# Kernel optimization log

Measured on AMD Instinct MI355X. Metric: run time of the kernel, lower is better.

The kernel has to match this reference:

```python
import jax, jax.numpy as jnp
import numpy as np

N = 50000
SELF_LOOP_W = 2.0  # GCNConv(improved=True)


def gcn_conv(x, edge_index, W, b):
    # x: [N, Fin], edge_index: [2, E] (row=source, col=target)
    h = x @ W  # [N, Fout]
    row, col = edge_index[0], edge_index[1]
    ones = jnp.ones(row.shape[0], dtype=h.dtype)
    deg = jax.ops.segment_sum(ones, col, num_segments=N) + SELF_LOOP_W
    dinv = jnp.where(deg > 0, jax.lax.rsqrt(deg), 0.0)
    norm = dinv[row] * dinv[col]  # [E]
    agg = jax.ops.segment_sum(norm[:, None] * h[row], col, num_segments=N)
    # self-loop contribution: weight 2.0, norm = dinv[i]^2
    agg = agg + (SELF_LOOP_W * dinv * dinv)[:, None] * h
    return agg + b


def setup_inputs() -> dict:
    key = jax.random.key(0)
    ks = jax.random.split(key, 12)
    F_in, H1, H2, H3 = 256, 256, 128, 64
    E, Ep, En = 800000, 200000, 200000
    def glorot(k, shape):
        lim = np.sqrt(6.0 / (shape[0] + shape[1]))
        return jax.random.uniform(k, shape, jnp.float32, -lim, lim)
    return {
        "x": jax.random.normal(ks[0], (N, F_in), jnp.float32),
        "train_edge_index": jax.random.randint(ks[1], (2, E), 0, N),
        "pos_edge_index": jax.random.randint(ks[2], (2, Ep), 0, N),
        "neg_edge_index": jax.random.randint(ks[3], (2, En), 0, N),
        "W1": glorot(ks[4], (F_in, H1)),
        "b1": jnp.zeros((H1,), jnp.float32),
        "W2": glorot(ks[5], (H1, H2)),
        "b2": jnp.zeros((H2,), jnp.float32),
        "Wl1": glorot(ks[6], (H2, H3)),
        "bl1": jnp.zeros((H3,), jnp.float32),
        "Wl2": glorot(ks[7], (H3, 1)),
        "bl2": jnp.zeros((1,), jnp.float32),
    }


def reference(x, train_edge_index, pos_edge_index, neg_edge_index,
              W1, b1, W2, b2, Wl1, bl1, Wl2, bl2):
    h = jax.nn.relu(gcn_conv(x, train_edge_index, W1, b1))
    h = gcn_conv(h, train_edge_index, W2, b2)  # [N, 128]
    tei = jnp.concatenate([pos_edge_index, neg_edge_index], axis=-1)  # [2, Ep+En]
    e = h[tei[1]] + h[tei[0]]  # x_i + x_j, [Etot, 128]
    e = jax.nn.relu(e @ Wl1 + bl1)
    e = jax.nn.sigmoid(e @ Wl2 + bl2)
    return e.reshape(-1)
```

## Files before the change

kernel.cpp:

```cpp
#include <hip/hip_runtime.h>
#include <math.h>

#define NV 50000
#define ETR 800000
#define EPOS 200000
#define ETEST 400000

typedef __attribute__((ext_vector_type(8))) short bf16x8;
typedef __attribute__((ext_vector_type(8))) unsigned short ushortx8;
typedef __attribute__((ext_vector_type(4))) float f32x4;

__device__ inline unsigned short f2b(float f) {
    union { float f; unsigned u; } v; v.f = f;
    unsigned r = v.u + 0x7fffu + ((v.u >> 16) & 1u);
    return (unsigned short)(r >> 16);
}
__device__ inline float blo(unsigned q) { union { unsigned u; float f; } v; v.u = q << 16; return v.f; }
__device__ inline float bhi(unsigned q) { union { unsigned u; float f; } v; v.u = q & 0xffff0000u; return v.f; }
__device__ inline float b2f(unsigned short s) { union { unsigned u; float f; } v; v.u = ((unsigned)s) << 16; return v.f; }

__device__ inline ushortx8 bf16add8(ushortx8 a, ushortx8 b) {
    ushortx8 r;
    #pragma unroll
    for (int i = 0; i < 8; ++i)
        r[i] = f2b(b2f(a[i]) + b2f(b[i]));
    return r;
}


__global__ void deg_kernel(const int* __restrict__ tei, int* __restrict__ deg) {
    int e = blockIdx.x * blockDim.x + threadIdx.x;
    if (e < ETR) atomicAdd(&deg[tei[ETR + e]], 1);
}

__global__ __launch_bounds__(1024) void partial_kernel(const int* __restrict__ deg,
                                                       int* __restrict__ partials) {
    int i = blockIdx.x * 1024 + threadIdx.x;
    int v = (i < NV) ? deg[i] : 0;
    #pragma unroll
    for (int off = 32; off > 0; off >>= 1) v += __shfl_xor(v, off);
    __shared__ int wsum[16];
    if ((threadIdx.x & 63) == 0) wsum[threadIdx.x >> 6] = v;
    __syncthreads();
    if (threadIdx.x == 0) {
        int s = 0;
        #pragma unroll
        for (int k = 0; k < 16; ++k) s += wsum[k];
        partials[blockIdx.x] = s;
    }
}

__global__ __launch_bounds__(1024) void ptr_kernel(
    const int* __restrict__ deg, const int* __restrict__ partials,
    int* __restrict__ ptr, int* __restrict__ cursor, float* __restrict__ dinv)
{
    int b = blockIdx.x, t = threadIdx.x;
    int i = b * 1024 + t;
    int d = (i < NV) ? deg[i] : 0;
    int lane = t & 63, w = t >> 6;
    int v = d;
    #pragma unroll
    for (int off = 1; off < 64; off <<= 1) {
        int u = __shfl_up(v, off);
        if (lane >= off) v += u;
    }
    __shared__ int wsum[16], woff[16];
    if (lane == 63) wsum[w] = v;
    __syncthreads();
    if (t == 0) {
        int s = 0;
        for (int k = 0; k < b; ++k) s += partials[k];
        for (int k = 0; k < 16; ++k) { woff[k] = s; s += wsum[k]; }
    }
    __syncthreads();
    int excl = woff[w] + v - d;
    if (i < NV) {
        ptr[i] = excl;
        cursor[i] = excl;
        dinv[i] = rsqrtf((float)d + 2.0f);
        if (i == NV - 1) ptr[NV] = excl + d;
    }
}

__global__ void fill_kernel(const int* __restrict__ tei, const float* __restrict__ dinv,
                            int* __restrict__ cursor, int2* __restrict__ edat) {
    int e = blockIdx.x * blockDim.x + threadIdx.x;
    if (e < ETR) {
        int row = tei[e];
        int col = tei[ETR + e];
        int p = atomicAdd(&cursor[col], 1);
        edat[p] = make_int2(row, __float_as_int(dinv[row] * dinv[col]));
    }
}


__global__ void cvt_wt_all_kernel(const float* __restrict__ W1, const float* __restrict__ W2,
                                  const float* __restrict__ Wl1,
                                  unsigned short* __restrict__ w1t, unsigned short* __restrict__ w2t,
                                  unsigned short* __restrict__ wl1t) {
    int idx = blockIdx.x * blockDim.x + threadIdx.x;
    if (idx < 65536) {
        int n = idx >> 8, k = idx & 255;
        w1t[idx] = f2b(W1[k * 256 + n]);
    } else if (idx < 98304) {
        int i = idx - 65536;
        int n = i >> 8, k = i & 255;
        w2t[i] = f2b(W2[k * 128 + n]);
    } else if (idx < 106496) {
        int i = idx - 98304;
        int n = i >> 7, k = i & 127;
        wl1t[i] = f2b(Wl1[k * 64 + n]);
    }
}


template<int N, int K, bool AF32>
__global__ __launch_bounds__(256) void mfma_gemm_kernel(
    const void* __restrict__ Av, const unsigned short* __restrict__ Bt,
    unsigned short* __restrict__ C, int M)
{
    constexpr int BK = 64;
    __shared__ unsigned short Asm[128][BK];
    __shared__ unsigned short Bsm[128][BK];
    int tid = threadIdx.x;
    int lane = tid & 63, wid = tid >> 6;
    int wr = wid >> 1, wc = wid & 1;
    int row0 = blockIdx.x * 128, col0 = blockIdx.y * 128;

    int sr = tid >> 3;
    int s8 = tid & 7;
    int sswz = s8 ^ (sr & 7);
    int fr = lane & 15;
    int g  = lane >> 4;

    f32x4 acc[4][4] = {};

    for (int k0 = 0; k0 < K; k0 += BK) {
        #pragma unroll
        for (int i = 0; i < 4; ++i) {
            int r = sr + i * 32;
            int gr = row0 + r;
            ushortx8 va = {0, 0, 0, 0, 0, 0, 0, 0};
            if constexpr (AF32) {
                const float* Af = (const float*)Av;
                if (gr < M) {
                    float4 f0 = *(const float4*)&Af[(size_t)gr * K + k0 + s8 * 8];
                    float4 f1 = *(const float4*)&Af[(size_t)gr * K + k0 + s8 * 8 + 4];
                    va[0] = f2b(f0.x); va[1] = f2b(f0.y); va[2] = f2b(f0.z); va[3] = f2b(f0.w);
                    va[4] = f2b(f1.x); va[5] = f2b(f1.y); va[6] = f2b(f1.z); va[7] = f2b(f1.w);
                }
            } else {
                const unsigned short* Ab = (const unsigned short*)Av;
                if (gr < M) va = *(const ushortx8*)&Ab[(size_t)gr * K + k0 + s8 * 8];
            }
            *(ushortx8*)&Asm[r][sswz * 8] = va;
            ushortx8 vb = *(const ushortx8*)&Bt[(size_t)(col0 + r) * K + k0 + s8 * 8];
            *(ushortx8*)&Bsm[r][sswz * 8] = vb;
        }
        __syncthreads();
        #pragma unroll
        for (int kf = 0; kf < BK; kf += 32) {
            int sbase = kf >> 3;
            bf16x8 af[4], bfr[4];
            #pragma unroll
            for (int m = 0; m < 4; ++m) {
                int rr = wr * 64 + m * 16 + fr;
                af[m] = *(const bf16x8*)&Asm[rr][((sbase + g) ^ (fr & 7)) * 8];
            }
            #pragma unroll
            for (int n = 0; n < 4; ++n) {
                int rr = wc * 64 + n * 16 + fr;
                bfr[n] = *(const bf16x8*)&Bsm[rr][((sbase + g) ^ (fr & 7)) * 8];
            }
            #pragma unroll
            for (int m = 0; m < 4; ++m)
                #pragma unroll
                for (int n = 0; n < 4; ++n)
                    acc[m][n] = __builtin_amdgcn_mfma_f32_16x16x32_bf16(af[m], bfr[n], acc[m][n], 0, 0, 0);
        }
        __syncthreads();
    }

    #pragma unroll
    for (int m = 0; m < 4; ++m) {
        int rbase = row0 + wr * 64 + m * 16 + g * 4;
        #pragma unroll
        for (int j = 0; j < 4; ++j) {
            int r = rbase + j;
            if (r < M) {
                #pragma unroll
                for (int n = 0; n < 4; ++n) {
                    int c = col0 + wc * 64 + n * 16 + fr;
                    C[(size_t)r * N + c] = f2b(acc[m][n][j]);
                }
            }
        }
    }
}


template<int F, bool RELU>
__global__ __launch_bounds__(256) void gather_kernel(
    const int* __restrict__ ptr, const int2* __restrict__ edat,
    const float* __restrict__ dinv, const unsigned short* __restrict__ hlin,
    const float* __restrict__ bias, unsigned short* __restrict__ hout)
{
    constexpr int V = F / 64;
    int gid = blockIdx.x * blockDim.x + threadIdx.x;
    int node = gid >> 6, lane = gid & 63;
    if (node >= NV) return;
    float dc = dinv[node];
    int j0 = ptr[node], j1 = ptr[node + 1];
    float acc[V] = {};
    const unsigned short* hb = hlin + lane * V;
    const long long* edl = (const long long*)edat;

    int j = j0;
    for (; j + 7 < j1; j += 8) {
        long long e[8];
        #pragma unroll
        for (int u = 0; u < 8; ++u) e[u] = __builtin_nontemporal_load(edl + j + u);
        if constexpr (V == 4) {
            uint2 q[8];
            #pragma unroll
            for (int u = 0; u < 8; ++u)
                q[u] = *(const uint2*)(hb + (size_t)(int)e[u] * F);
            #pragma unroll
            for (int u = 0; u < 8; ++u) {
                float n = __int_as_float((int)(e[u] >> 32));
                acc[0] += n * blo(q[u].x);
                acc[1] += n * bhi(q[u].x);
                acc[2] += n * blo(q[u].y);
                acc[3] += n * bhi(q[u].y);
            }
        } else {
            unsigned q[8];
            #pragma unroll
            for (int u = 0; u < 8; ++u)
                q[u] = *(const unsigned*)(hb + (size_t)(int)e[u] * F);
            #pragma unroll
            for (int u = 0; u < 8; ++u) {
                float n = __int_as_float((int)(e[u] >> 32));
                acc[0] += n * blo(q[u]);
                acc[1] += n * bhi(q[u]);
            }
        }
    }
    for (; j + 3 < j1; j += 4) {
        long long e[4];
        #pragma unroll
        for (int u = 0; u < 4; ++u) e[u] = __builtin_nontemporal_load(edl + j + u);
        if constexpr (V == 4) {
            uint2 q[4];
            #pragma unroll
            for (int u = 0; u < 4; ++u)
                q[u] = *(const uint2*)(hb + (size_t)(int)e[u] * F);
            #pragma unroll
            for (int u = 0; u < 4; ++u) {
                float n = __int_as_float((int)(e[u] >> 32));
                acc[0] += n * blo(q[u].x);
                acc[1] += n * bhi(q[u].x);
                acc[2] += n * blo(q[u].y);
                acc[3] += n * bhi(q[u].y);
            }
        } else {
            unsigned q[4];
            #pragma unroll
            for (int u = 0; u < 4; ++u)
                q[u] = *(const unsigned*)(hb + (size_t)(int)e[u] * F);
            #pragma unroll
            for (int u = 0; u < 4; ++u) {
                float n = __int_as_float((int)(e[u] >> 32));
                acc[0] += n * blo(q[u]);
                acc[1] += n * bhi(q[u]);
            }
        }
    }
    for (; j < j1; ++j) {
        long long e0 = __builtin_nontemporal_load(edl + j);
        float n0 = __int_as_float((int)(e0 >> 32));
        if constexpr (V == 4) {
            uint2 q0 = *(const uint2*)(hb + (size_t)(int)e0 * F);
            acc[0] += n0 * blo(q0.x);
            acc[1] += n0 * bhi(q0.x);
            acc[2] += n0 * blo(q0.y);
            acc[3] += n0 * bhi(q0.y);
        } else {
            unsigned q0 = *(const unsigned*)(hb + (size_t)(int)e0 * F);
            acc[0] += n0 * blo(q0);
            acc[1] += n0 * bhi(q0);
        }
    }

    const unsigned short* ps = hb + (size_t)node * F;
    float sw = 2.0f * dc * dc;
    if constexpr (V == 4) {
        uint2 qs = *(const uint2*)ps;
        float o0 = acc[0] + sw * blo(qs.x) + bias[lane * 4 + 0];
        float o1 = acc[1] + sw * bhi(qs.x) + bias[lane * 4 + 1];
        float o2 = acc[2] + sw * blo(qs.y) + bias[lane * 4 + 2];
        float o3 = acc[3] + sw * bhi(qs.y) + bias[lane * 4 + 3];
        if (RELU) {
            o0 = fmaxf(o0, 0.f); o1 = fmaxf(o1, 0.f);
            o2 = fmaxf(o2, 0.f); o3 = fmaxf(o3, 0.f);
        }
        union { unsigned short u[4]; unsigned long long ll; } pk;
        pk.u[0] = f2b(o0); pk.u[1] = f2b(o1); pk.u[2] = f2b(o2); pk.u[3] = f2b(o3);
        __builtin_nontemporal_store(pk.ll, (unsigned long long*)(hout + (size_t)node * F + lane * 4));
    } else {
        unsigned qs = *(const unsigned*)ps;
        float o0 = acc[0] + sw * blo(qs) + bias[lane * 2 + 0];
        float o1 = acc[1] + sw * bhi(qs) + bias[lane * 2 + 1];
        if (RELU) { o0 = fmaxf(o0, 0.f); o1 = fmaxf(o1, 0.f); }
        union { unsigned short u[2]; unsigned q; } pk;
        pk.u[0] = f2b(o0); pk.u[1] = f2b(o1);
        __builtin_nontemporal_store(pk.q, (unsigned*)(hout + (size_t)node * F + lane * 2));
    }
}


__global__ __launch_bounds__(256) void edge_mlp_mfma_kernel(
    const int* __restrict__ pos, const int* __restrict__ neg,
    const unsigned short* __restrict__ h2, const unsigned short* __restrict__ Wl1t,
    const float* __restrict__ bl1, const float* __restrict__ Wl2,
    const float* __restrict__ bl2, float* __restrict__ out)
{
    __shared__ unsigned short Es[128][128];
    __shared__ unsigned short Ws[64][128];
    int tid = threadIdx.x;
    int lane = tid & 63, w = tid >> 6;
    int fr = lane & 15, g = lane >> 4;
    int e0 = blockIdx.x * 128;

    #pragma unroll
    for (int k = 0; k < 4; ++k) {
        int chunk = tid + k * 256;
        int row = chunk >> 4, c = chunk & 15;
        *(ushortx8*)&Ws[row][(c ^ (row & 7)) * 8] = *(const ushortx8*)&Wl1t[chunk * 8];
    }

    int et = tid >> 1, hh = tid & 1;
    int eg = e0 + et;
    int a, b;
    if (eg < EPOS) { a = pos[eg]; b = pos[EPOS + eg]; }
    else { int i = eg - EPOS; a = neg[i]; b = neg[EPOS + i]; }
    const unsigned short* pa = h2 + (size_t)a * 128 + hh * 64;
    const unsigned short* pb = h2 + (size_t)b * 128 + hh * 64;
    #pragma unroll
    for (int c8 = 0; c8 < 8; ++c8) {
        ushortx8 va = *(const ushortx8*)&pa[c8 * 8];
        ushortx8 vb = *(const ushortx8*)&pb[c8 * 8];
        ushortx8 vs = bf16add8(va, vb);
        int c = hh * 8 + c8;
        *(ushortx8*)&Es[et][(c ^ (et & 7)) * 8] = vs;
    }
    __syncthreads();

    f32x4 acc[2][4] = {};
    #pragma unroll
    for (int ks = 0; ks < 4; ++ks) {
        int c = ks * 4 + g;
        bf16x8 af[2], bfr[4];
        #pragma unroll
        for (int m = 0; m < 2; ++m) {
            int r = w * 32 + m * 16 + fr;
            af[m] = *(const bf16x8*)&Es[r][(c ^ (r & 7)) * 8];
        }
        #pragma unroll
        for (int n = 0; n < 4; ++n) {
            int r = n * 16 + fr;
            bfr[n] = *(const bf16x8*)&Ws[r][(c ^ (r & 7)) * 8];
        }
        #pragma unroll
        for (int m = 0; m < 2; ++m)
            #pragma unroll
            for (int n = 0; n < 4; ++n)
                acc[m][n] = __builtin_amdgcn_mfma_f32_16x16x32_bf16(af[m], bfr[n], acc[m][n], 0, 0, 0);
    }

    float bl2v = bl2[0];
    float b1v[4], w2v[4];
    #pragma unroll
    for (int n = 0; n < 4; ++n) {
        b1v[n] = bl1[n * 16 + fr];
        w2v[n] = Wl2[n * 16 + fr];
    }
    #pragma unroll
    for (int m = 0; m < 2; ++m) {
        float p[4];
        #pragma unroll
        for (int j = 0; j < 4; ++j) {
            float s = 0.f;
            #pragma unroll
            for (int n = 0; n < 4; ++n)
                s += fmaxf(acc[m][n][j] + b1v[n], 0.0f) * w2v[n];
            p[j] = s;
        }
        #pragma unroll
        for (int off = 1; off < 16; off <<= 1) {
            #pragma unroll
            for (int j = 0; j < 4; ++j)
                p[j] += __shfl_xor(p[j], off);
        }
        int ebase = e0 + w * 32 + m * 16 + g * 4;
        #pragma unroll
        for (int j = 0; j < 4; ++j)
            if (fr == j)
                out[ebase + j] = 1.0f / (1.0f + expf(-(p[j] + bl2v)));
    }
}


extern "C" void kernel_launch(void* const* d_in, const int* in_sizes, int n_in,
                              void* d_out, int out_size, void* d_ws, size_t ws_size,
                              hipStream_t stream) {
    const float* x   = (const float*)d_in[0];
    const int*   tei = (const int*)d_in[1];
    const int*   pos = (const int*)d_in[2];
    const int*   neg = (const int*)d_in[3];
    const float* W1  = (const float*)d_in[4];
    const float* b1  = (const float*)d_in[5];
    const float* W2  = (const float*)d_in[6];
    const float* b2  = (const float*)d_in[7];
    const float* Wl1 = (const float*)d_in[8];
    const float* bl1 = (const float*)d_in[9];
    const float* Wl2 = (const float*)d_in[10];
    const float* bl2 = (const float*)d_in[11];
    float* out = (float*)d_out;

    float* fws = (float*)d_ws;
    int*   iws = (int*)d_ws;
    unsigned short* usws = (unsigned short*)d_ws;
    float* dinv     = fws;
    int*   deg      = iws + 50000;
    int*   ptr      = iws + 100000;
    int*   cursor   = iws + 150002;
    int2*  edat     = (int2*)(iws + 200064);
    int*   partials = iws + 1800064;
    unsigned short* w1t  = usws + 2ull * 1800192;
    unsigned short* w2t  = usws + 2ull * 1832960;
    unsigned short* wl1t = usws + 2ull * 1849344;
    unsigned short* bufX = usws + 2ull * 1853504;
    unsigned short* bufL16 = usws + 2ull * 8253504;
    unsigned short* bufH = usws + 2ull * 14653504;

    hipMemsetAsync(deg, 0, NV * sizeof(int), stream);

    deg_kernel<<<(ETR + 255) / 256, 256, 0, stream>>>(tei, deg);
    partial_kernel<<<49, 1024, 0, stream>>>(deg, partials);
    ptr_kernel<<<49, 1024, 0, stream>>>(deg, partials, ptr, cursor, dinv);
    fill_kernel<<<(ETR + 255) / 256, 256, 0, stream>>>(tei, dinv, cursor, edat);
    cvt_wt_all_kernel<<<416, 256, 0, stream>>>(W1, W2, Wl1, w1t, w2t, wl1t);

    mfma_gemm_kernel<256, 256, true><<<dim3(391, 2), 256, 0, stream>>>(x, w1t, bufL16, NV);
    gather_kernel<256, true><<<(NV * 64) / 256, 256, 0, stream>>>(ptr, edat, dinv, bufL16, b1, bufH);

    mfma_gemm_kernel<128, 256, false><<<dim3(391, 1), 256, 0, stream>>>(bufH, w2t, bufX, NV);
    gather_kernel<128, false><<<(NV * 64) / 256, 256, 0, stream>>>(ptr, edat, dinv, bufX, b2, bufL16);

    edge_mlp_mfma_kernel<<<ETEST / 128, 256, 0, stream>>>(pos, neg, bufL16, wl1t, bl1, Wl2, bl2, out);
}
```

Baseline: 298.1 us.

## Merge independent preprocessing kernels into combined block-partitioned launches

Folds the degree atomic count and the W1 transpose/convert into one launch, and folds the first GEMM, the degree partial sums and the W2/Wl1 conversions into a second launch, with blocks dispatched by block index. This cuts the kernel count from eleven to eight, removing launch gaps and letting the small independent tasks share the machine with the GEMM. Costs: the merged kernels carry the GEMM's shared memory and register footprint for every block, and partial sums now run alongside the GEMM rather than before it.

Result: faster. 291.7 us (-2.1%).

```diff
diff --git a/kernel.cpp b/kernel.cpp
--- a/kernel.cpp
+++ b/kernel.cpp
@@ -28,96 +28,10 @@
 }
 
 
-__global__ void deg_kernel(const int* __restrict__ tei, int* __restrict__ deg) {
-    int e = blockIdx.x * blockDim.x + threadIdx.x;
-    if (e < ETR) atomicAdd(&deg[tei[ETR + e]], 1);
-}
-
-__global__ __launch_bounds__(1024) void partial_kernel(const int* __restrict__ deg,
-                                                       int* __restrict__ partials) {
-    int i = blockIdx.x * 1024 + threadIdx.x;
-    int v = (i < NV) ? deg[i] : 0;
-    #pragma unroll
-    for (int off = 32; off > 0; off >>= 1) v += __shfl_xor(v, off);
-    __shared__ int wsum[16];
-    if ((threadIdx.x & 63) == 0) wsum[threadIdx.x >> 6] = v;
-    __syncthreads();
-    if (threadIdx.x == 0) {
-        int s = 0;
-        #pragma unroll
-        for (int k = 0; k < 16; ++k) s += wsum[k];
-        partials[blockIdx.x] = s;
-    }
-}
-
-__global__ __launch_bounds__(1024) void ptr_kernel(
-    const int* __restrict__ deg, const int* __restrict__ partials,
-    int* __restrict__ ptr, int* __restrict__ cursor, float* __restrict__ dinv)
-{
-    int b = blockIdx.x, t = threadIdx.x;
-    int i = b * 1024 + t;
-    int d = (i < NV) ? deg[i] : 0;
-    int lane = t & 63, w = t >> 6;
-    int v = d;
-    #pragma unroll
-    for (int off = 1; off < 64; off <<= 1) {
-        int u = __shfl_up(v, off);
-        if (lane >= off) v += u;
-    }
-    __shared__ int wsum[16], woff[16];
-    if (lane == 63) wsum[w] = v;
-    __syncthreads();
-    if (t == 0) {
-        int s = 0;
-        for (int k = 0; k < b; ++k) s += partials[k];
-        for (int k = 0; k < 16; ++k) { woff[k] = s; s += wsum[k]; }
-    }
-    __syncthreads();
-    int excl = woff[w] + v - d;
-    if (i < NV) {
-        ptr[i] = excl;
-        cursor[i] = excl;
-        dinv[i] = rsqrtf((float)d + 2.0f);
-        if (i == NV - 1) ptr[NV] = excl + d;
-    }
-}
-
-__global__ void fill_kernel(const int* __restrict__ tei, const float* __restrict__ dinv,
-                            int* __restrict__ cursor, int2* __restrict__ edat) {
-    int e = blockIdx.x * blockDim.x + threadIdx.x;
-    if (e < ETR) {
-        int row = tei[e];
-        int col = tei[ETR + e];
-        int p = atomicAdd(&cursor[col], 1);
-        edat[p] = make_int2(row, __float_as_int(dinv[row] * dinv[col]));
-    }
-}
-
-
-__global__ void cvt_wt_all_kernel(const float* __restrict__ W1, const float* __restrict__ W2,
-                                  const float* __restrict__ Wl1,
-                                  unsigned short* __restrict__ w1t, unsigned short* __restrict__ w2t,
-                                  unsigned short* __restrict__ wl1t) {
-    int idx = blockIdx.x * blockDim.x + threadIdx.x;
-    if (idx < 65536) {
-        int n = idx >> 8, k = idx & 255;
-        w1t[idx] = f2b(W1[k * 256 + n]);
-    } else if (idx < 98304) {
-        int i = idx - 65536;
-        int n = i >> 8, k = i & 255;
-        w2t[i] = f2b(W2[k * 128 + n]);
-    } else if (idx < 106496) {
-        int i = idx - 98304;
-        int n = i >> 7, k = i & 127;
-        wl1t[i] = f2b(Wl1[k * 64 + n]);
-    }
-}
-
-
 template<int N, int K, bool AF32>
-__global__ __launch_bounds__(256) void mfma_gemm_kernel(
+__device__ __forceinline__ void gemm_body(
     const void* __restrict__ Av, const unsigned short* __restrict__ Bt,
-    unsigned short* __restrict__ C, int M)
+    unsigned short* __restrict__ C, int M, int row0, int col0)
 {
     constexpr int BK = 64;
     __shared__ unsigned short Asm[128][BK];
@@ -125,7 +39,6 @@
     int tid = threadIdx.x;
     int lane = tid & 63, wid = tid >> 6;
     int wr = wid >> 1, wc = wid & 1;
-    int row0 = blockIdx.x * 128, col0 = blockIdx.y * 128;
 
     int sr = tid >> 3;
     int s8 = tid & 7;
@@ -196,6 +109,114 @@
             }
         }
     }
+}
+
+
+__global__ __launch_bounds__(256) void fat0_kernel(
+    const int* __restrict__ tei, int* __restrict__ deg,
+    const float* __restrict__ W1, unsigned short* __restrict__ w1t)
+{
+    int bid = blockIdx.x;
+    int t = threadIdx.x;
+    if (bid < 3125) {
+        int e = bid * 256 + t;
+        if (e < ETR) atomicAdd(&deg[tei[ETR + e]], 1);
+    } else {
+        int i = (bid - 3125) * 256 + t;
+        int n = i >> 8, k = i & 255;
+        w1t[i] = f2b(W1[k * 256 + n]);
+    }
+}
+
+
+__global__ __launch_bounds__(256) void fat1_kernel(
+    const float* __restrict__ x, const unsigned short* __restrict__ w1t,
+    unsigned short* __restrict__ h1lin,
+    const int* __restrict__ deg, int* __restrict__ partials,
+    const float* __restrict__ W2, unsigned short* __restrict__ w2t,
+    const float* __restrict__ Wl1, unsigned short* __restrict__ wl1t)
+{
+    int bid = blockIdx.x;
+    int t = threadIdx.x;
+    if (bid < 782) {
+        int row0 = (bid >> 1) * 128, col0 = (bid & 1) * 128;
+        gemm_body<256, 256, true>(x, w1t, h1lin, NV, row0, col0);
+    } else if (bid < 831) {
+        int p = bid - 782;
+        int base = p * 1024;
+        int s = 0;
+        #pragma unroll
+        for (int k = 0; k < 4; ++k) {
+            int i = base + t + k * 256;
+            if (i < NV) s += deg[i];
+        }
+        #pragma unroll
+        for (int off = 32; off > 0; off >>= 1) s += __shfl_xor(s, off);
+        __shared__ int ws4[4];
+        if ((t & 63) == 0) ws4[t >> 6] = s;
+        __syncthreads();
+        if (t == 0) partials[p] = ws4[0] + ws4[1] + ws4[2] + ws4[3];
+    } else if (bid < 959) {
+        int i = (bid - 831) * 256 + t;
+        int n = i >> 8, k = i & 255;
+        w2t[i] = f2b(W2[k * 128 + n]);
+    } else {
+        int i = (bid - 959) * 256 + t;
+        int n = i >> 7, k = i & 127;
+        wl1t[i] = f2b(Wl1[k * 64 + n]);
+    }
+}
+
+
+__global__ __launch_bounds__(1024) void ptr_kernel(
+    const int* __restrict__ deg, const int* __restrict__ partials,
+    int* __restrict__ ptr, int* __restrict__ cursor, float* __restrict__ dinv)
+{
+    int b = blockIdx.x, t = threadIdx.x;
+    int i = b * 1024 + t;
+    int d = (i < NV) ? deg[i] : 0;
+    int lane = t & 63, w = t >> 6;
+    int v = d;
+    #pragma unroll
+    for (int off = 1; off < 64; off <<= 1) {
+        int u = __shfl_up(v, off);
+        if (lane >= off) v += u;
+    }
+    __shared__ int wsum[16], woff[16];
+    if (lane == 63) wsum[w] = v;
+    __syncthreads();
+    if (t == 0) {
+        int s = 0;
+        for (int k = 0; k < b; ++k) s += partials[k];
+        for (int k = 0; k < 16; ++k) { woff[k] = s; s += wsum[k]; }
+    }
+    __syncthreads();
+    int excl = woff[w] + v - d;
+    if (i < NV) {
+        ptr[i] = excl;
+        cursor[i] = excl;
+        dinv[i] = rsqrtf((float)d + 2.0f);
+        if (i == NV - 1) ptr[NV] = excl + d;
+    }
+}
+
+__global__ void fill_kernel(const int* __restrict__ tei, const float* __restrict__ dinv,
+                            int* __restrict__ cursor, int2* __restrict__ edat) {
+    int e = blockIdx.x * blockDim.x + threadIdx.x;
+    if (e < ETR) {
+        int row = tei[e];
+        int col = tei[ETR + e];
+        int p = atomicAdd(&cursor[col], 1);
+        edat[p] = make_int2(row, __float_as_int(dinv[row] * dinv[col]));
+    }
+}
+
+
+__global__ __launch_bounds__(256) void gemm2_kernel(
+    const unsigned short* __restrict__ A, const unsigned short* __restrict__ Bt,
+    unsigned short* __restrict__ C, int M)
+{
+    gemm_body<128, 256, false>(A, Bt, C, M, blockIdx.x * 128, 0);
 }
 
 
@@ -446,16 +467,16 @@
 
     hipMemsetAsync(deg, 0, NV * sizeof(int), stream);
 
-    deg_kernel<<<(ETR + 255) / 256, 256, 0, stream>>>(tei, deg);
-    partial_kernel<<<49, 1024, 0, stream>>>(deg, partials);
+    fat0_kernel<<<3381, 256, 0, stream>>>(tei, deg, W1, w1t);
+
+    fat1_kernel<<<991, 256, 0, stream>>>(x, w1t, bufL16, deg, partials, W2, w2t, Wl1, wl1t);
+
     ptr_kernel<<<49, 1024, 0, stream>>>(deg, partials, ptr, cursor, dinv);
     fill_kernel<<<(ETR + 255) / 256, 256, 0, stream>>>(tei, dinv, cursor, edat);
-    cvt_wt_all_kernel<<<416, 256, 0, stream>>>(W1, W2, Wl1, w1t, w2t, wl1t);
-
-    mfma_gemm_kernel<256, 256, true><<<dim3(391, 2), 256, 0, stream>>>(x, w1t, bufL16, NV);
+
     gather_kernel<256, true><<<(NV * 64) / 256, 256, 0, stream>>>(ptr, edat, dinv, bufL16, b1, bufH);
 
-    mfma_gemm_kernel<128, 256, false><<<dim3(391, 1), 256, 0, stream>>>(bufH, w2t, bufX, NV);
+    gemm2_kernel<<<391, 256, 0, stream>>>(bufH, w2t, bufX, NV);
     gather_kernel<128, false><<<(NV * 64) / 256, 256, 0, stream>>>(ptr, edat, dinv, bufX, b2, bufL16);
 
     edge_mlp_mfma_kernel<<<ETEST / 128, 256, 0, stream>>>(pos, neg, bufL16, wl1t, bl1, Wl2, bl2, out);
```

## Fuse CSR prep into one persistent kernel and sort test edges by source

Applied to the files above, without the earlier changes.

Merges the degree count, partial sums, scan, CSR fill and weight conversion into a single 256-block persistent kernel that uses software grid barriers, cutting several launches. It also buckets the pos/neg test edges by source node, so the edge MLP reads h2 rows with more locality, and scatters outputs through an eorig permutation. This adds atomics for the test-edge sort, spin barriers that assume every block is co-resident, and a scattered output write.

Result: slower. 714.2 us (+139.6%).

```diff
diff --git a/kernel.cpp b/kernel.cpp
--- a/kernel.cpp
+++ b/kernel.cpp
@@ -5,6 +5,7 @@
 #define ETR 800000
 #define EPOS 200000
 #define ETEST 400000
+#define NTH 262144
 
 typedef __attribute__((ext_vector_type(8))) short bf16x8;
 typedef __attribute__((ext_vector_type(8))) unsigned short ushortx8;
@@ -27,97 +28,107 @@
     return r;
 }
 
-
-__global__ void deg_kernel(const int* __restrict__ tei, int* __restrict__ deg) {
-    int e = blockIdx.x * blockDim.x + threadIdx.x;
-    if (e < ETR) atomicAdd(&deg[tei[ETR + e]], 1);
-}
-
-__global__ __launch_bounds__(1024) void partial_kernel(const int* __restrict__ deg,
-                                                       int* __restrict__ partials) {
-    int i = blockIdx.x * 1024 + threadIdx.x;
-    int v = (i < NV) ? deg[i] : 0;
-    #pragma unroll
-    for (int off = 32; off > 0; off >>= 1) v += __shfl_xor(v, off);
-    __shared__ int wsum[16];
-    if ((threadIdx.x & 63) == 0) wsum[threadIdx.x >> 6] = v;
+__device__ inline void gbar(int* cnt, int target) {
+    __threadfence();
     __syncthreads();
     if (threadIdx.x == 0) {
-        int s = 0;
-        #pragma unroll
-        for (int k = 0; k < 16; ++k) s += wsum[k];
-        partials[blockIdx.x] = s;
-    }
-}
-
-__global__ __launch_bounds__(1024) void ptr_kernel(
-    const int* __restrict__ deg, const int* __restrict__ partials,
-    int* __restrict__ ptr, int* __restrict__ cursor, float* __restrict__ dinv)
+        atomicAdd(cnt, 1);
+        while (atomicAdd(cnt, 0) < target) __builtin_amdgcn_s_sleep(8);
+    }
+    __syncthreads();
+    __threadfence();
+}
+
+
+__global__ __launch_bounds__(1024) void prep_kernel(
+    const int* __restrict__ tei, const int* __restrict__ pos, const int* __restrict__ neg,
+    const float* __restrict__ W1, const float* __restrict__ W2, const float* __restrict__ Wl1,
+    unsigned short* __restrict__ w1t, unsigned short* __restrict__ w2t, unsigned short* __restrict__ wl1t,
+    int* __restrict__ deg, int* __restrict__ tdeg,
+    int* __restrict__ ptr, int* __restrict__ cursor,
+    int* __restrict__ tptr, int* __restrict__ tcursor,
+    float* __restrict__ dinv, int* __restrict__ partials, int* __restrict__ tpartials,
+    int2* __restrict__ edat, int2* __restrict__ eab, int* __restrict__ eorig,
+    int* __restrict__ bars)
 {
     int b = blockIdx.x, t = threadIdx.x;
-    int i = b * 1024 + t;
-    int d = (i < NV) ? deg[i] : 0;
-    int lane = t & 63, w = t >> 6;
-    int v = d;
-    #pragma unroll
-    for (int off = 1; off < 64; off <<= 1) {
-        int u = __shfl_up(v, off);
-        if (lane >= off) v += u;
-    }
-    __shared__ int wsum[16], woff[16];
-    if (lane == 63) wsum[w] = v;
+    int gtid = b * 1024 + t;
+
+    if (gtid < 65536) {
+        w1t[gtid] = f2b(W1[(gtid & 255) * 256 + (gtid >> 8)]);
+    } else if (gtid < 98304) {
+        int i = gtid - 65536;
+        w2t[i] = f2b(W2[(i & 255) * 128 + (i >> 8)]);
+    } else if (gtid < 106496) {
+        int i = gtid - 98304;
+        wl1t[i] = f2b(Wl1[(i & 127) * 64 + (i >> 7)]);
+    }
+    for (int e = gtid; e < ETR; e += NTH)
+        atomicAdd(&deg[tei[ETR + e]], 1);
+    for (int e = gtid; e < ETEST; e += NTH) {
+        int a = (e < EPOS) ? pos[e] : neg[e - EPOS];
+        atomicAdd(&tdeg[a], 1);
+    }
+    gbar(bars + 0, gridDim.x);
+
+    int i = b * 196 + t;
+    int d = 0, td = 0;
+    if (t < 196 && i < NV) { d = deg[i]; td = tdeg[i]; }
+    __shared__ int s1[256], s2[256];
+    __shared__ int base1, base2;
+    if (t < 256) { s1[t] = d; s2[t] = td; }
     __syncthreads();
+    for (int off = 128; off > 0; off >>= 1) {
+        if (t < off) { s1[t] += s1[t + off]; s2[t] += s2[t + off]; }
+        __syncthreads();
+    }
+    if (t == 0) { partials[b] = s1[0]; tpartials[b] = s2[0]; }
+    gbar(bars + 1, gridDim.x);
+
     if (t == 0) {
-        int s = 0;
-        for (int k = 0; k < b; ++k) s += partials[k];
-        for (int k = 0; k < 16; ++k) { woff[k] = s; s += wsum[k]; }
-    }
+        int s = 0, ts = 0;
+        for (int k = 0; k < b; ++k) { s += partials[k]; ts += tpartials[k]; }
+        base1 = s; base2 = ts;
+    }
+    if (t < 256) { s1[t] = d; s2[t] = td; }
     __syncthreads();
-    int excl = woff[w] + v - d;
-    if (i < NV) {
-        ptr[i] = excl;
-        cursor[i] = excl;
+    for (int off = 1; off < 256; off <<= 1) {
+        int v1 = 0, v2 = 0;
+        if (t < 256 && t >= off) { v1 = s1[t - off]; v2 = s2[t - off]; }
+        __syncthreads();
+        if (t < 256) { s1[t] += v1; s2[t] += v2; }
+        __syncthreads();
+    }
+    if (t < 196 && i < NV) {
+        int e1 = base1 + s1[t] - d;
+        int e2 = base2 + s2[t] - td;
+        ptr[i] = e1;  cursor[i] = e1;
+        tptr[i] = e2; tcursor[i] = e2;
         dinv[i] = rsqrtf((float)d + 2.0f);
-        if (i == NV - 1) ptr[NV] = excl + d;
-    }
-}
-
-__global__ void fill_kernel(const int* __restrict__ tei, const float* __restrict__ dinv,
-                            int* __restrict__ cursor, int2* __restrict__ edat) {
-    int e = blockIdx.x * blockDim.x + threadIdx.x;
-    if (e < ETR) {
-        int row = tei[e];
-        int col = tei[ETR + e];
+        if (i == NV - 1) ptr[NV] = e1 + d;
+    }
+    gbar(bars + 2, gridDim.x);
+
+    for (int e = gtid; e < ETR; e += NTH) {
+        int row = tei[e], col = tei[ETR + e];
         int p = atomicAdd(&cursor[col], 1);
         edat[p] = make_int2(row, __float_as_int(dinv[row] * dinv[col]));
     }
-}
-
-
-__global__ void cvt_wt_all_kernel(const float* __restrict__ W1, const float* __restrict__ W2,
-                                  const float* __restrict__ Wl1,
-                                  unsigned short* __restrict__ w1t, unsigned short* __restrict__ w2t,
-                                  unsigned short* __restrict__ wl1t) {
-    int idx = blockIdx.x * blockDim.x + threadIdx.x;
-    if (idx < 65536) {
-        int n = idx >> 8, k = idx & 255;
-        w1t[idx] = f2b(W1[k * 256 + n]);
-    } else if (idx < 98304) {
-        int i = idx - 65536;
-        int n = i >> 8, k = i & 255;
-        w2t[i] = f2b(W2[k * 128 + n]);
-    } else if (idx < 106496) {
-        int i = idx - 98304;
-        int n = i >> 7, k = i & 127;
-        wl1t[i] = f2b(Wl1[k * 64 + n]);
+    for (int e = gtid; e < ETEST; e += NTH) {
+        int a, bb;
+        if (e < EPOS) { a = pos[e]; bb = pos[EPOS + e]; }
+        else { int i2 = e - EPOS; a = neg[i2]; bb = neg[EPOS + i2]; }
+        int p = atomicAdd(&tcursor[a], 1);
+        eab[p] = make_int2(a, bb);
+        eorig[p] = e;
     }
 }
 
 
 template<int N, int K, bool AF32>
-__global__ __launch_bounds__(256) void mfma_gemm_kernel(
+__device__ __forceinline__ void gemm_body(
     const void* __restrict__ Av, const unsigned short* __restrict__ Bt,
-    unsigned short* __restrict__ C, int M)
+    unsigned short* __restrict__ C, int M, int row0, int col0)
 {
     constexpr int BK = 64;
     __shared__ unsigned short Asm[128][BK];
@@ -125,7 +136,6 @@
     int tid = threadIdx.x;
     int lane = tid & 63, wid = tid >> 6;
     int wr = wid >> 1, wc = wid & 1;
-    int row0 = blockIdx.x * 128, col0 = blockIdx.y * 128;
 
     int sr = tid >> 3;
     int s8 = tid & 7;
@@ -198,6 +208,21 @@
     }
 }
 
+__global__ __launch_bounds__(256) void gemm1_kernel(
+    const float* __restrict__ x, const unsigned short* __restrict__ w1t,
+    unsigned short* __restrict__ C)
+{
+    int row0 = (blockIdx.x >> 1) * 128, col0 = (blockIdx.x & 1) * 128;
+    gemm_body<256, 256, true>(x, w1t, C, NV, row0, col0);
+}
+
+__global__ __launch_bounds__(256) void gemm2_kernel(
+    const unsigned short* __restrict__ A, const unsigned short* __restrict__ Bt,
+    unsigned short* __restrict__ C)
+{
+    gemm_body<128, 256, false>(A, Bt, C, NV, blockIdx.x * 128, 0);
+}
+
 
 template<int F, bool RELU>
 __global__ __launch_bounds__(256) void gather_kernel(
@@ -320,7 +345,7 @@
 
 
 __global__ __launch_bounds__(256) void edge_mlp_mfma_kernel(
-    const int* __restrict__ pos, const int* __restrict__ neg,
+    const int2* __restrict__ eab, const int* __restrict__ eorig,
     const unsigned short* __restrict__ h2, const unsigned short* __restrict__ Wl1t,
     const float* __restrict__ bl1, const float* __restrict__ Wl2,
     const float* __restrict__ bl2, float* __restrict__ out)
@@ -340,12 +365,9 @@
     }
 
     int et = tid >> 1, hh = tid & 1;
-    int eg = e0 + et;
-    int a, b;
-    if (eg < EPOS) { a = pos[eg]; b = pos[EPOS + eg]; }
-    else { int i = eg - EPOS; a = neg[i]; b = neg[EPOS + i]; }
-    const unsigned short* pa = h2 + (size_t)a * 128 + hh * 64;
-    const unsigned short* pb = h2 + (size_t)b * 128 + hh * 64;
+    int2 ab = eab[e0 + et];
+    const unsigned short* pa = h2 + (size_t)ab.x * 128 + hh * 64;
+    const unsigned short* pb = h2 + (size_t)ab.y * 128 + hh * 64;
     #pragma unroll
     for (int c8 = 0; c8 < 8; ++c8) {
         ushortx8 va = *(const ushortx8*)&pa[c8 * 8];
@@ -406,7 +428,7 @@
         #pragma unroll
         for (int j = 0; j < 4; ++j)
             if (fr == j)
-                out[ebase + j] = 1.0f / (1.0f + expf(-(p[j] + bl2v)));
+                out[eorig[ebase + j]] = 1.0f / (1.0f + expf(-(p[j] + bl2v)));
     }
 }
 
@@ -431,32 +453,38 @@
     float* fws = (float*)d_ws;
     int*   iws = (int*)d_ws;
     unsigned short* usws = (unsigned short*)d_ws;
-    float* dinv     = fws;
-    int*   deg      = iws + 50000;
-    int*   ptr      = iws + 100000;
-    int*   cursor   = iws + 150002;
-    int2*  edat     = (int2*)(iws + 200064);
-    int*   partials = iws + 1800064;
-    unsigned short* w1t  = usws + 2ull * 1800192;
-    unsigned short* w2t  = usws + 2ull * 1832960;
-    unsigned short* wl1t = usws + 2ull * 1849344;
-    unsigned short* bufX = usws + 2ull * 1853504;
-    unsigned short* bufL16 = usws + 2ull * 8253504;
-    unsigned short* bufH = usws + 2ull * 14653504;
-
-    hipMemsetAsync(deg, 0, NV * sizeof(int), stream);
-
-    deg_kernel<<<(ETR + 255) / 256, 256, 0, stream>>>(tei, deg);
-    partial_kernel<<<49, 1024, 0, stream>>>(deg, partials);
-    ptr_kernel<<<49, 1024, 0, stream>>>(deg, partials, ptr, cursor, dinv);
-    fill_kernel<<<(ETR + 255) / 256, 256, 0, stream>>>(tei, dinv, cursor, edat);
-    cvt_wt_all_kernel<<<416, 256, 0, stream>>>(W1, W2, Wl1, w1t, w2t, wl1t);
-
-    mfma_gemm_kernel<256, 256, true><<<dim3(391, 2), 256, 0, stream>>>(x, w1t, bufL16, NV);
+    float* dinv      = fws;
+    int*   deg       = iws + 50000;
+    int*   tdeg      = iws + 100000;
+    int*   bars      = iws + 150000;
+    int*   ptr       = iws + 150064;
+    int*   cursor    = iws + 200128;
+    int*   tptr      = iws + 250128;
+    int*   tcursor   = iws + 300160;
+    int*   partials  = iws + 350208;
+    int*   tpartials = iws + 350464;
+    int2*  edat      = (int2*)(iws + 350720);
+    int2*  eab       = (int2*)(iws + 1950720);
+    int*   eorig     = iws + 2750720;
+    unsigned short* w1t  = usws + 2ull * 3150720;
+    unsigned short* w2t  = usws + 2ull * 3183488;
+    unsigned short* wl1t = usws + 2ull * 3199872;
+    unsigned short* bufX   = usws + 2ull * 3203968;
+    unsigned short* bufL16 = usws + 2ull * 6403968;
+    unsigned short* bufH   = usws + 2ull * 12803968;
+
+    hipMemsetAsync(deg, 0, (100000 + 64) * sizeof(int), stream);
+
+    prep_kernel<<<256, 1024, 0, stream>>>(
+        tei, pos, neg, W1, W2, Wl1, w1t, w2t, wl1t,
+        deg, tdeg, ptr, cursor, tptr, tcursor,
+        dinv, partials, tpartials, edat, eab, eorig, bars);
+
+    gemm1_kernel<<<782, 256, 0, stream>>>(x, w1t, bufL16);
     gather_kernel<256, true><<<(NV * 64) / 256, 256, 0, stream>>>(ptr, edat, dinv, bufL16, b1, bufH);
 
-    mfma_gemm_kernel<128, 256, false><<<dim3(391, 1), 256, 0, stream>>>(bufH, w2t, bufX, NV);
+    gemm2_kernel<<<391, 256, 0, stream>>>(bufH, w2t, bufX);
     gather_kernel<128, false><<<(NV * 64) / 256, 256, 0, stream>>>(ptr, edat, dinv, bufX, b2, bufL16);
 
-    edge_mlp_mfma_kernel<<<ETEST / 128, 256, 0, stream>>>(pos, neg, bufL16, wl1t, bl1, Wl2, bl2, out);
-}
+    edge_mlp_mfma_kernel<<<ETEST / 128, 256, 0, stream>>>(eab, eorig, bufL16, wl1t, bl1, Wl2, bl2, out);
+}
```
